# Performance work log

Measured on AMD Instinct MI355X. Metric: run time of the kernel, lower is better.

## Reference

```python
import jax, jax.numpy as jnp
import numpy as np

B, CIN, COUT, H, W_SP = 16, 128, 128, 56, 56
E, KH, KW = 4, 3, 3

def setup_inputs() -> dict:
    key = jax.random.key(0)
    k1, k2, k3 = jax.random.split(key, 3)
    x = jax.random.normal(k1, (B, CIN, H, W_SP), dtype=jnp.float32)
    routing_weights = jax.random.uniform(k2, (B, E), dtype=jnp.float32)
    # expert conv kernels, OIHW, stacked over experts: [E, COUT, CIN, KH, KW]
    W = jax.random.normal(k3, (E, COUT, CIN, KH, KW), dtype=jnp.float32) * 0.05
    return {"x": x, "routing_weights": routing_weights, "W": W}

def reference(x, routing_weights, W):
    # Each expert: full Conv2d(stride=1, padding=1, dilation=1, groups=1, no bias)
    def one_expert(w):  # w: [COUT, CIN, KH, KW]
        return jax.lax.conv_general_dilated(
            x, w,
            window_strides=(1, 1),
            padding=((1, 1), (1, 1)),
            dimension_numbers=("NCHW", "OIHW", "NCHW"),
        )
    expert_outs = jax.vmap(one_expert)(W)  # [E, B, COUT, H, W]
    # per-sample scalar mix: sum_e routing[b, e] * expert_outs[e, b]
    out = jnp.einsum("ebchw,be->bchw", expert_outs, routing_weights)
    return out
```

## Files before the change

### kernel.cpp

```cpp
#include <hip/hip_runtime.h>


typedef float  f32x16 __attribute__((ext_vector_type(16)));
typedef short  s16x8  __attribute__((ext_vector_type(8)));
typedef unsigned short u16;

#define CIN   128
#define COUT  128
#define HH    56
#define WW    56
#define SP    (HH*WW)
#define EW    147456
#define BW_   147456
#define XSTR  72
#define XB    (4*66*XSTR)
#define AB    8192

static __device__ __forceinline__ u16 f2bf(float f) {
    unsigned u = __builtin_bit_cast(unsigned, f);
    return (u16)((u + 0x7FFFu + ((u >> 16) & 1u)) >> 16);
}

static __device__ __forceinline__ void gload16(const void* g, void* l) {
    __builtin_amdgcn_global_load_lds(
        (const __attribute__((address_space(1))) void*)g,
        (__attribute__((address_space(3))) void*)l, 16, 0, 0);
}

__global__ __launch_bounds__(256) void mix_kernel(const float* __restrict__ W,
                                                  const float* __restrict__ r,
                                                  u16* __restrict__ Wmix) {
    const int o  = blockIdx.x * 256 + threadIdx.x;
    const int ci = o & 127;
    const int co = o >> 7;
    const int cc   = ci >> 5;
    const int ci_l = ci & 31;
    const int bq   = blockIdx.y;

    float wv[4][9];
    const float* src = W + ((size_t)co * CIN + ci) * 9;
    #pragma unroll
    for (int e = 0; e < 4; ++e)
        #pragma unroll
        for (int tap = 0; tap < 9; ++tap)
            wv[e][tap] = src[(size_t)e * EW + tap];

    #pragma unroll
    for (int bb = 0; bb < 4; ++bb) {
        const int b = bq * 4 + bb;
        const float r0 = r[b*4+0], r1 = r[b*4+1], r2 = r[b*4+2], r3 = r[b*4+3];
        #pragma unroll
        for (int tap = 0; tap < 9; ++tap) {
            float acc = r0*wv[0][tap] + r1*wv[1][tap]
                      + r2*wv[2][tap] + r3*wv[3][tap];
            Wmix[(size_t)b * BW_ + (((cc*9 + tap)*128 + co) << 5) + ci_l] = f2bf(acc);
        }
    }
}

__global__ __launch_bounds__(512, 4) void conv_mfma(const float* __restrict__ x,
                                                    const u16* __restrict__ Wmix,
                                                    float* __restrict__ out) {
    __shared__ __align__(16) char ldsb[XB + 4*AB];

    const int bid = blockIdx.x;
    const int bs  = (bid & 7) * 56 + (bid >> 3);
    const int b   = bs / 28;
    const int ph  = bs % 28;
    const int t    = threadIdx.x;
    const int lane = t & 63;
    const int wid  = t >> 6;
    const int wm   = (wid >> 2) & 1;
    const int wn   = (wid >> 1) & 1;
    const int wp   = wid & 1;
    const int l31  = lane & 31;
    const int khalf= lane >> 5;

    const u16*   WmixB = Wmix + (size_t)b * BW_;
    const float* xbB   = x + (size_t)b * CIN * SP;

    const int ssl = (t & 3) ^ ((t >> 3) & 3);

    f32x16 acc[2];
    acc[0] = (f32x16)0.f;
    acc[1] = (f32x16)0.f;

    auto stageA = [&](int it) {
        char* ldst = ldsb + XB + (it & 3) * AB + wid * 1024;
        const u16* ga = WmixB + it * 4096 + (t >> 2) * 32 + ssl * 8;
        gload16(ga, ldst);
    };

    auto stageX = [&](int cc) {
        #pragma unroll
        for (int i = 0; i < 2; ++i) {
            int slot = i * 512 + t;
            int c    = 1 + (slot & 63);
            int row  = (slot >> 6) & 3;
            int g    = slot >> 8;
            int rr   = 2*ph - 1 + row;
            int w    = c - 1;
            bool ok  = ((unsigned)rr < 56u) && (w < 56);
            const float* p = xbB + (size_t)(cc*32 + g*8) * SP + rr*56 + w;
            s16x8 v;
            #pragma unroll
            for (int j = 0; j < 8; ++j) {
                float f = ok ? p[(size_t)j * SP] : 0.f;
                v[j] = (short)f2bf(f);
            }
            *(s16x8*)(ldsb + (row*66 + c)*XSTR + g*16) = v;
        }
    };

    auto compute = [&](int it, int kh, int kw) {
        const char* Ab = ldsb + XB + (it & 3) * AB;
        #pragma unroll
        for (int ksub = 0; ksub < 2; ++ksub) {
            const int s = ksub * 2 + khalf;
            s16x8 af[2], bv;
            #pragma unroll
            for (int mf = 0; mf < 2; ++mf)
                af[mf] = *(const s16x8*)(Ab + (wm*64 + mf*32 + l31)*64
                                            + ((s ^ ((l31 >> 1) & 3)) * 16));
            const int c = wp*32 + l31 + kw;
            bv = *(const s16x8*)(ldsb + ((wn + kh)*66 + c)*XSTR + s*16);
            #pragma unroll
            for (int mf = 0; mf < 2; ++mf)
                acc[mf] = __builtin_amdgcn_mfma_f32_32x32x16_bf16(
                    af[mf], bv, acc[mf], 0, 0, 0);
        }
    };

    if (t < 32) {
        int row = t >> 3, col = ((t >> 2) & 1) ? 65 : 0, sl = t & 3;
        *(s16x8*)(ldsb + (row*66 + col)*XSTR + sl*16) = (s16x8)0;
    }
    stageA(0);
    stageA(1);
    stageX(0);
    asm volatile("s_waitcnt lgkmcnt(0)" ::: "memory");
    __builtin_amdgcn_sched_barrier(0);
    __builtin_amdgcn_s_barrier();
    __builtin_amdgcn_sched_barrier(0);

    #pragma unroll
    for (int cc = 0; cc < 4; ++cc) {
        if (cc) {
            __builtin_amdgcn_sched_barrier(0);
            __builtin_amdgcn_s_barrier();
            __builtin_amdgcn_sched_barrier(0);
            stageX(cc);
            asm volatile("s_waitcnt lgkmcnt(0)" ::: "memory");
            __builtin_amdgcn_sched_barrier(0);
            __builtin_amdgcn_s_barrier();
            __builtin_amdgcn_sched_barrier(0);
        }
        #pragma unroll
        for (int tap = 0; tap < 9; ++tap) {
            const int it = cc * 9 + tap;
            if (it + 2 < 36) {
                stageA(it + 2);
                asm volatile("s_waitcnt vmcnt(2)" ::: "memory");
            } else if (it + 1 < 36) {
                asm volatile("s_waitcnt vmcnt(1)" ::: "memory");
            } else {
                asm volatile("s_waitcnt vmcnt(0)" ::: "memory");
            }
            __builtin_amdgcn_s_barrier();
            __builtin_amdgcn_sched_barrier(0);
            __builtin_amdgcn_s_setprio(1);
            compute(it, tap / 3, tap % 3);
            __builtin_amdgcn_s_setprio(0);
        }
    }

    const int w = wp * 32 + l31;
    if (w < 56) {
        const int hrow = 2 * ph + wn;
        #pragma unroll
        for (int mf = 0; mf < 2; ++mf) {
            #pragma unroll
            for (int rg = 0; rg < 16; ++rg) {
                int co = wm*64 + mf*32 + (rg & 3) + 8*(rg >> 2) + 4*khalf;
                out[(((size_t)b*COUT + co)*HH + hrow)*WW + w] = acc[mf][rg];
            }
        }
    }
}

extern "C" void kernel_launch(void* const* d_in, const int* in_sizes, int n_in,
                              void* d_out, int out_size, void* d_ws, size_t ws_size,
                              hipStream_t stream) {
    const float* x = (const float*)d_in[0];
    const float* r = (const float*)d_in[1];
    const float* W = (const float*)d_in[2];
    float* outp = (float*)d_out;
    u16* Wmix = (u16*)d_ws;

    mix_kernel<<<dim3(64, 4), 256, 0, stream>>>(W, r, Wmix);
    conv_mfma <<<448, 512, 0, stream>>>(x, Wmix, outp);
}
```

Measured before the change: 34.36 us.

## Split conv tiles along width into half-width blocks of 256 threads

```diff
diff --git a/kernel.cpp b/kernel.cpp
--- a/kernel.cpp
+++ b/kernel.cpp
@@ -13,7 +13,7 @@
 #define EW    147456
 #define BW_   147456
 #define XSTR  72
-#define XB    (4*66*XSTR)
+#define XB2   (4*34*XSTR)
 #define AB    8192
 
 static __device__ __forceinline__ u16 f2bf(float f) {
@@ -58,21 +58,23 @@
     }
 }
 
-__global__ __launch_bounds__(512, 4) void conv_mfma(const float* __restrict__ x,
+__global__ __launch_bounds__(256, 3) void conv_mfma(const float* __restrict__ x,
                                                     const u16* __restrict__ Wmix,
                                                     float* __restrict__ out) {
-    __shared__ __align__(16) char ldsb[XB + 4*AB];
+    __shared__ __align__(16) char ldsb[XB2 + 4*AB];
 
     const int bid = blockIdx.x;
-    const int bs  = (bid & 7) * 56 + (bid >> 3);
-    const int b   = bs / 28;
-    const int ph  = bs % 28;
+    const int bs  = (bid & 7) * 112 + (bid >> 3);
+    const int b   = bs / 56;
+    const int rem = bs % 56;
+    const int ph  = rem >> 1;
+    const int pxh = rem & 1;
+    const int w0  = pxh * 32;
     const int t    = threadIdx.x;
     const int lane = t & 63;
     const int wid  = t >> 6;
-    const int wm   = (wid >> 2) & 1;
-    const int wn   = (wid >> 1) & 1;
-    const int wp   = wid & 1;
+    const int wm   = wid >> 1;
+    const int wn   = wid & 1;
     const int l31  = lane & 31;
     const int khalf= lane >> 5;
 
@@ -86,34 +88,38 @@
     acc[1] = (f32x16)0.f;
 
     auto stageA = [&](int it) {
-        char* ldst = ldsb + XB + (it & 3) * AB + wid * 1024;
+        char* base = ldsb + XB2 + (it & 3) * AB;
         const u16* ga = WmixB + it * 4096 + (t >> 2) * 32 + ssl * 8;
-        gload16(ga, ldst);
+        gload16(ga,        base + wid * 1024);
+        gload16(ga + 2048, base + 4096 + wid * 1024);
     };
 
     auto stageX = [&](int cc) {
         #pragma unroll
-        for (int i = 0; i < 2; ++i) {
-            int slot = i * 512 + t;
-            int c    = 1 + (slot & 63);
-            int row  = (slot >> 6) & 3;
-            int g    = slot >> 8;
-            int rr   = 2*ph - 1 + row;
-            int w    = c - 1;
-            bool ok  = ((unsigned)rr < 56u) && (w < 56);
-            const float* p = xbB + (size_t)(cc*32 + g*8) * SP + rr*56 + w;
-            s16x8 v;
-            #pragma unroll
-            for (int j = 0; j < 8; ++j) {
-                float f = ok ? p[(size_t)j * SP] : 0.f;
-                v[j] = (short)f2bf(f);
+        for (int i = 0; i < 3; ++i) {
+            int s = i * 256 + t;
+            if (s < 544) {
+                int c    = s % 34;
+                int rest = s / 34;
+                int row  = rest & 3;
+                int g    = rest >> 2;
+                int rr   = 2*ph - 1 + row;
+                int w    = w0 + c - 1;
+                bool ok  = ((unsigned)rr < 56u) && ((unsigned)w < 56u);
+                const float* p = xbB + (size_t)(cc*32 + g*8) * SP + rr*56 + w;
+                s16x8 v;
+                #pragma unroll
+                for (int j = 0; j < 8; ++j) {
+                    float f = ok ? p[(size_t)j * SP] : 0.f;
+                    v[j] = (short)f2bf(f);
+                }
+                *(s16x8*)(ldsb + (row*34 + c)*XSTR + g*16) = v;
             }
-            *(s16x8*)(ldsb + (row*66 + c)*XSTR + g*16) = v;
         }
     };
 
     auto compute = [&](int it, int kh, int kw) {
-        const char* Ab = ldsb + XB + (it & 3) * AB;
+        const char* Ab = ldsb + XB2 + (it & 3) * AB;
         #pragma unroll
         for (int ksub = 0; ksub < 2; ++ksub) {
             const int s = ksub * 2 + khalf;
@@ -122,8 +128,8 @@
             for (int mf = 0; mf < 2; ++mf)
                 af[mf] = *(const s16x8*)(Ab + (wm*64 + mf*32 + l31)*64
                                             + ((s ^ ((l31 >> 1) & 3)) * 16));
-            const int c = wp*32 + l31 + kw;
-            bv = *(const s16x8*)(ldsb + ((wn + kh)*66 + c)*XSTR + s*16);
+            const int c = l31 + kw;
+            bv = *(const s16x8*)(ldsb + ((wn + kh)*34 + c)*XSTR + s*16);
             #pragma unroll
             for (int mf = 0; mf < 2; ++mf)
                 acc[mf] = __builtin_amdgcn_mfma_f32_32x32x16_bf16(
@@ -131,10 +137,6 @@
         }
     };
 
-    if (t < 32) {
-        int row = t >> 3, col = ((t >> 2) & 1) ? 65 : 0, sl = t & 3;
-        *(s16x8*)(ldsb + (row*66 + col)*XSTR + sl*16) = (s16x8)0;
-    }
     stageA(0);
     stageA(1);
     stageX(0);
@@ -160,9 +162,9 @@
             const int it = cc * 9 + tap;
             if (it + 2 < 36) {
                 stageA(it + 2);
+                asm volatile("s_waitcnt vmcnt(4)" ::: "memory");
+            } else if (it + 1 < 36) {
                 asm volatile("s_waitcnt vmcnt(2)" ::: "memory");
-            } else if (it + 1 < 36) {
-                asm volatile("s_waitcnt vmcnt(1)" ::: "memory");
             } else {
                 asm volatile("s_waitcnt vmcnt(0)" ::: "memory");
             }
@@ -174,7 +176,7 @@
         }
     }
 
-    const int w = wp * 32 + l31;
+    const int w = w0 + l31;
     if (w < 56) {
         const int hrow = 2 * ph + wn;
         #pragma unroll
@@ -198,5 +200,5 @@
     u16* Wmix = (u16*)d_ws;
 
     mix_kernel<<<dim3(64, 4), 256, 0, stream>>>(W, r, Wmix);
-    conv_mfma <<<448, 512, 0, stream>>>(x, Wmix, outp);
-}
+    conv_mfma <<<896, 256, 0, stream>>>(x, Wmix, outp);
+}
```

Measured after the change: 44.78 us. 30.3% more time.
